# Kernel optimization log

Hardware: AMD Instinct MI355X
Metric: run time of the kernel (lower is better)

Reference implementation:

```python
import jax, jax.numpy as jnp
from jax import lax
import numpy as np

EPS = 1e-5


def ref_points(Hk, Wk):
    # torch linspace(0.5, Hk-0.5, Hk)/Hk * 2 - 1, stacked (y, x)
    ys = (jnp.linspace(0.5, Hk - 0.5, Hk) / Hk) * 2.0 - 1.0
    xs = (jnp.linspace(0.5, Wk - 0.5, Wk) / Wk) * 2.0 - 1.0
    yy, xx = jnp.meshgrid(ys, xs, indexing='ij')
    return jnp.stack([yy, xx], axis=-1)  # (Hk, Wk, 2) in (y, x) order


def grid_sample(img, grid):
    # Bilinear, align_corners=True, zeros padding (torch F.grid_sample defaults).
    # img: (N, C, Hi, Wi); grid: (N, Hg, Wg, 2) with (x, y) in [-1, 1].
    N, C, Hi, Wi = img.shape
    Hg, Wg = grid.shape[1], grid.shape[2]
    gx = (grid[..., 0] + 1.0) * 0.5 * (Wi - 1)
    gy = (grid[..., 1] + 1.0) * 0.5 * (Hi - 1)
    x0 = jnp.floor(gx)
    y0 = jnp.floor(gy)
    wx1 = gx - x0
    wy1 = gy - y0
    imgf = img.reshape(N, C, Hi * Wi)

    def corner(ix, iy, w):
        valid = (ix >= 0) & (ix < Wi) & (iy >= 0) & (iy < Hi)
        idx = (jnp.clip(iy, 0, Hi - 1).astype(jnp.int32) * Wi
               + jnp.clip(ix, 0, Wi - 1).astype(jnp.int32)).reshape(N, -1)
        vals = jax.vmap(lambda im, f: im[:, f])(imgf, idx)  # (N, C, Hg*Wg)
        return vals * (w * valid).reshape(N, 1, -1)

    out = (corner(x0, y0, (1 - wx1) * (1 - wy1))
           + corner(x0 + 1, y0, wx1 * (1 - wy1))
           + corner(x0, y0 + 1, (1 - wx1) * wy1)
           + corner(x0 + 1, y0 + 1, wx1 * wy1))
    return out.reshape(N, C, Hg, Wg)


def setup_inputs() -> dict:
    key = jax.random.key(0)
    ks = jax.random.split(key, 8)
    B, C, H, W = 8, 128, 64, 64
    gc, nH = 64, 4
    return {
        'x': jax.random.normal(ks[0], (B, C, H, W), jnp.float32),
        'w_dw': jax.random.normal(ks[1], (gc, 1, 5, 5), jnp.float32) * 0.1,
        'ln_w': jnp.ones((gc,), jnp.float32),
        'w_off': jax.random.normal(ks[2], (3, gc), jnp.float32) * 0.1,
        'wq': jax.random.normal(ks[3], (C, C), jnp.float32) * 0.05,
        'wk': jax.random.normal(ks[4], (C, C), jnp.float32) * 0.05,
        'wv': jax.random.normal(ks[5], (C, C), jnp.float32) * 0.05,
        'wo': jax.random.normal(ks[6], (C, C), jnp.float32) * 0.05,
        'rpe': jax.random.normal(ks[7], (nH, 2 * H - 1, 2 * W - 1), jnp.float32) * 0.01,
    }


def reference(x, w_dw, ln_w, w_off, wq, wk, wv, wo, rpe):
    B, C, H, W = x.shape
    G, nH = 2, 4
    gc = C // G           # group channels
    dh = C // nH          # head channels
    gh = nH // G          # heads per group
    scale = dh ** -0.5
    orf = 1.0             # offset_range_factor

    conv1x1 = lambda t, w: jnp.einsum('oi,bihw->bohw', w, t)

    q = conv1x1(x, wq)                                    # (B, C, H, W)
    q_off = q.reshape(B * G, gc, H, W)

    # conv_offset: depthwise 5x5 stride 4 pad 2 -> BiasFree LN (over C) -> GELU -> 1x1 to 3
    off = lax.conv_general_dilated(q_off, w_dw, (4, 4), ((2, 2), (2, 2)),
                                   dimension_numbers=('NCHW', 'OIHW', 'NCHW'),
                                   feature_group_count=gc)  # (B*G, gc, Hk, Wk)
    var = jnp.var(off, axis=1, keepdims=True)
    off = off / jnp.sqrt(var + EPS) * ln_w.reshape(1, -1, 1, 1)
    off = jax.nn.gelu(off, approximate=False)
    off = jnp.einsum('oi,bihw->bohw', w_off, off)          # (B*G, 3, Hk, Wk)

    Hk, Wk = off.shape[2], off.shape[3]
    n = Hk * Wk

    # channel 0 = y offset, channel 1 = x offset, channel 2 = modulation
    offset = jnp.stack([jnp.tanh(off[:, 0]) * (orf / Hk),
                        jnp.tanh(off[:, 1]) * (orf / Wk)], axis=-1)  # (B*G, Hk, Wk, 2) (y,x)
    dm = jax.nn.sigmoid(off[:, 2])[:, None]                # (B*G, 1, Hk, Wk)

    pos = offset + ref_points(Hk, Wk)[None]                # (B*G, Hk, Wk, 2) (y,x)

    xs = grid_sample(x.reshape(B * G, gc, H, W), pos[..., ::-1])  # grid in (x,y)
    xs = (xs * dm).reshape(B, C, 1, n)

    k = conv1x1(xs, wk).reshape(B * nH, dh, n)
    v = conv1x1(xs, wv).reshape(B * nH, dh, n)
    qf = q.reshape(B * nH, dh, H * W)

    attn = jnp.einsum('bcm,bcn->bmn', qf, k) * scale       # (B*nH, H*W, n)

    # relative-position bias sampled at continuous displacements
    rpe_b = jnp.broadcast_to(rpe[None], (B, nH, 2 * H - 1, 2 * W - 1)
                             ).reshape(B * G, gh, 2 * H - 1, 2 * W - 1)
    qg = ref_points(H, W).reshape(H * W, 2)                # (H*W, 2)
    disp = (qg[None, :, None, :] - pos.reshape(B * G, 1, n, 2)) * 0.5  # (B*G, H*W, n, 2)
    bias = grid_sample(rpe_b, disp[..., ::-1]).reshape(B * nH, H * W, n)

    attn = jax.nn.softmax(attn + bias, axis=2)
    out = jnp.einsum('bmn,bcn->bcm', attn, v).reshape(B, C, H, W)
    return conv1x1(out, wo)
```

## Files before the change

### kernel.cpp

```cpp
#include <hip/hip_runtime.h>
#include <hip/hip_bf16.h>
#include <math.h>

#define HW 4096
#define NCH 128

typedef __attribute__((ext_vector_type(8))) short short8;
typedef __attribute__((ext_vector_type(4))) float f32x4;
typedef __attribute__((ext_vector_type(4))) unsigned u32x4;

__device__ __forceinline__ short f2bf(float f) {
  union { __hip_bfloat16 h; short s; } u;
  u.h = __float2bfloat16(f);
  return u.s;
}
__device__ __forceinline__ float bf2f(short s) {
  union { unsigned u; float f; } u;
  u.u = ((unsigned)(unsigned short)s) << 16;
  return u.f;
}

__global__ __launch_bounds__(256) void xq_kernel(
    const float* __restrict__ x, const float* __restrict__ wq,
    const float* __restrict__ wk, const float* __restrict__ wv,
    const float* __restrict__ wo, const float* __restrict__ rpe,
    short* __restrict__ xT, float* __restrict__ qT,
    short* __restrict__ wk_bf, short* __restrict__ wv_bf,
    short* __restrict__ wo_bf, unsigned* __restrict__ tab) {
  __shared__ float s[128][65];
  int tid = threadIdx.x;
  if (blockIdx.y >= 8) {
    int id = (blockIdx.y - 8) * 64 + blockIdx.x;
    if (id < 64) {
      int i = id * 256 + tid;
      wk_bf[i] = f2bf(wk[i]);
      wv_bf[i] = f2bf(wv[i]);
      wo_bf[i] = f2bf(wo[i]);
    } else {
      int i = (id - 64) * 256 + tid;
      int h = i >> 14, r = i & 16383;
      int row = r >> 7, col = r & 127;
      float lo = 0.f, hi = 0.f;
      if (col < 127) {
        if (row >= 1) lo = rpe[h * 16129 + (row - 1) * 127 + col];
        if (row < 127) hi = rpe[h * 16129 + row * 127 + col];
      }
      union { unsigned u; _Float16 h2[2]; } pk;
      pk.h2[0] = (_Float16)(lo * 1.4426950408889634f);
      pk.h2[1] = (_Float16)((hi - lo) * 1.4426950408889634f);
      tab[i] = pk.u;
    }
    return;
  }
  int b = blockIdx.y;
  int m0 = blockIdx.x * 64;
  {
    int ml = tid & 63, ch = tid >> 6;
#pragma unroll
    for (int i = 0; i < 32; ++i) {
      int c = i * 4 + ch;
      s[c][ml] = x[((size_t)(b * NCH + c)) * HW + m0 + ml];
    }
  }
  __syncthreads();
  {
    int c = tid & 127, mh = tid >> 7;
#pragma unroll
    for (int i = 0; i < 32; ++i) {
      int m = i * 2 + mh;
      xT[((size_t)(b * HW + m0 + m)) * NCH + c] = f2bf(s[c][m]);
    }
  }
  int w = tid >> 6, lane = tid & 63, l15 = lane & 15, qd = lane >> 4;
  int mrow = w * 16 + l15;
  f32x4 acc[8];
#pragma unroll
  for (int ot = 0; ot < 8; ++ot) acc[ot] = (f32x4){0.f, 0.f, 0.f, 0.f};
#pragma unroll
  for (int kc = 0; kc < 4; ++kc) {
    short8 ah, al;
#pragma unroll
    for (int j = 0; j < 8; ++j) {
      float v = s[kc * 32 + qd * 8 + j][mrow];
      short hi = f2bf(v);
      ah[j] = hi;
      al[j] = f2bf(v - bf2f(hi));
    }
#pragma unroll
    for (int ot = 0; ot < 8; ++ot) {
      const float* wr = wq + (size_t)(ot * 16 + l15) * NCH + kc * 32 + qd * 8;
      f32x4 w0 = *(const f32x4*)wr;
      f32x4 w1 = *(const f32x4*)(wr + 4);
      short8 bh, bl;
#pragma unroll
      for (int j = 0; j < 4; ++j) {
        short h0 = f2bf(w0[j]);
        bh[j] = h0;
        bl[j] = f2bf(w0[j] - bf2f(h0));
        short h1 = f2bf(w1[j]);
        bh[4 + j] = h1;
        bl[4 + j] = f2bf(w1[j] - bf2f(h1));
      }
      acc[ot] = __builtin_amdgcn_mfma_f32_16x16x32_bf16(ah, bh, acc[ot], 0, 0, 0);
      acc[ot] = __builtin_amdgcn_mfma_f32_16x16x32_bf16(al, bh, acc[ot], 0, 0, 0);
      acc[ot] = __builtin_amdgcn_mfma_f32_16x16x32_bf16(ah, bl, acc[ot], 0, 0, 0);
    }
  }
#pragma unroll
  for (int ot = 0; ot < 8; ++ot)
#pragma unroll
    for (int r = 0; r < 4; ++r)
      qT[((size_t)(b * HW + m0 + w * 16 + qd * 4 + r)) * NCH + ot * 16 + l15] =
          acc[ot][r];
}

__device__ __forceinline__ float wsum64(float v) {
#pragma unroll
  for (int o = 32; o > 0; o >>= 1) v += __shfl_xor(v, o);
  return v;
}

__global__ __launch_bounds__(256) void conv_offset_kernel(
    const float* __restrict__ qT, const float* __restrict__ w_dw,
    const float* __restrict__ ln_w, const float* __restrict__ w_off,
    float* __restrict__ pos, float* __restrict__ dm) {
  int tid = threadIdx.x;
  int c = tid & 63;
  int p = blockIdx.x * 4 + (tid >> 6);
  int bg = blockIdx.y;
  int py = p >> 4, px = p & 15;
  const float* qp = qT + (size_t)(bg >> 1) * HW * NCH + (bg & 1) * 64 + c;
  const float* wd = w_dw + c * 25;
  float acc = 0.f;
#pragma unroll
  for (int ky = 0; ky < 5; ++ky) {
    int iy = 4 * py + ky - 2;
    if (iy < 0 || iy >= 64) continue;
#pragma unroll
    for (int kx = 0; kx < 5; ++kx) {
      int ix = 4 * px + kx - 2;
      if (ix < 0 || ix >= 64) continue;
      acc += wd[ky * 5 + kx] * qp[(size_t)(iy * 64 + ix) * NCH];
    }
  }
  float mean = wsum64(acc) * (1.f / 64.f);
  float msq = wsum64(acc * acc) * (1.f / 64.f);
  float var = msq - mean * mean;
  float g = acc * rsqrtf(var + 1e-5f) * ln_w[c];
  g = 0.5f * g * (1.f + erff(g * 0.70710678118654752f));
  float o0 = wsum64(w_off[c] * g);
  float o1 = wsum64(w_off[64 + c] * g);
  float o2 = wsum64(w_off[128 + c] * g);
  if (c == 0) {
    int idx = bg * 256 + p;
    pos[idx * 2] = tanhf(o0) * (1.f / 16.f) + ((py + 0.5f) * (1.f / 8.f) - 1.f);
    pos[idx * 2 + 1] = tanhf(o1) * (1.f / 16.f) + ((px + 0.5f) * (1.f / 8.f) - 1.f);
    dm[idx] = 1.f / (1.f + expf(-o2));
  }
}

__global__ __launch_bounds__(256) void sample_xs_kernel(
    const short* __restrict__ xT, const float* __restrict__ pos,
    const float* __restrict__ dm, short* __restrict__ xsT) {
  int tid = threadIdx.x;
  int c = tid & 63;
  int p = blockIdx.y * 4 + (tid >> 6);
  int bg = blockIdx.x;
  int b = bg >> 1, ch0 = (bg & 1) * 64;
  int idx = bg * 256 + p;
  float posy = pos[idx * 2], posx = pos[idx * 2 + 1];
  float dmv = dm[idx];
  float gx = (posx + 1.f) * 31.5f;
  float gy = (posy + 1.f) * 31.5f;
  float x0f = floorf(gx), y0f = floorf(gy);
  int ix = (int)x0f, iy = (int)y0f;
  float fx = gx - x0f, fy = gy - y0f;
  float w00 = (1.f - fx) * (1.f - fy), w10 = fx * (1.f - fy);
  float w01 = (1.f - fx) * fy, w11 = fx * fy;
  bool vx0 = (ix >= 0 && ix < 64), vx1 = (ix + 1 >= 0 && ix + 1 < 64);
  bool vy0 = (iy >= 0 && iy < 64), vy1 = (iy + 1 >= 0 && iy + 1 < 64);
  if (!(vx0 && vy0)) w00 = 0.f;
  if (!(vx1 && vy0)) w10 = 0.f;
  if (!(vx0 && vy1)) w01 = 0.f;
  if (!(vx1 && vy1)) w11 = 0.f;
  int x0c = min(max(ix, 0), 63), x1c = min(max(ix + 1, 0), 63);
  int y0c = min(max(iy, 0), 63), y1c = min(max(iy + 1, 0), 63);
  size_t rb = (size_t)b * HW * NCH + ch0 + c;
  float v = w00 * bf2f(xT[rb + (size_t)(y0c * 64 + x0c) * NCH]) +
            w10 * bf2f(xT[rb + (size_t)(y0c * 64 + x1c) * NCH]) +
            w01 * bf2f(xT[rb + (size_t)(y1c * 64 + x0c) * NCH]) +
            w11 * bf2f(xT[rb + (size_t)(y1c * 64 + x1c) * NCH]);
  xsT[((size_t)(b * 256 + p)) * NCH + ch0 + c] = f2bf(v * dmv);
}

__global__ __launch_bounds__(256) void kv_mfma_kernel(
    const short* __restrict__ xsT, const short* __restrict__ wk_bf,
    const short* __restrict__ wv_bf, short* __restrict__ kbf,
    short* __restrict__ vbf) {
  int tid = threadIdx.x;
  int w = tid >> 6, lane = tid & 63, l15 = lane & 15, qd = lane >> 4;
  int bh = blockIdx.x, b = bh >> 2;
  int n0 = blockIdx.y * 64 + w * 16;
  f32x4 acc[2];
  acc[0] = (f32x4){0.f, 0.f, 0.f, 0.f};
  acc[1] = (f32x4){0.f, 0.f, 0.f, 0.f};

  size_t xrow = ((size_t)(b * 256 + n0 + l15)) * NCH + qd * 8;
  if (blockIdx.z == 0) {
#pragma unroll
    for (int kc = 0; kc < 4; ++kc) {
      short8 a = *(const short8*)&xsT[xrow + kc * 32];
#pragma unroll
      for (int ot = 0; ot < 2; ++ot) {
        short8 bb = *(const short8*)&wk_bf[(size_t)((bh & 3) * 32 + ot * 16 + l15) * NCH + kc * 32 + qd * 8];
        acc[ot] = __builtin_amdgcn_mfma_f32_16x16x32_bf16(a, bb, acc[ot], 0, 0, 0);
      }
    }
#pragma unroll
    for (int ot = 0; ot < 2; ++ot)
#pragma unroll
      for (int r = 0; r < 4; ++r)
        kbf[((size_t)(bh * 256 + n0 + qd * 4 + r)) * 32 + ot * 16 + l15] =
            f2bf(acc[ot][r]);
  } else {
#pragma unroll
    for (int kc = 0; kc < 4; ++kc) {
      short8 bb = *(const short8*)&xsT[xrow + kc * 32];
#pragma unroll
      for (int ot = 0; ot < 2; ++ot) {
        short8 a = *(const short8*)&wv_bf[(size_t)((bh & 3) * 32 + ot * 16 + l15) * NCH + kc * 32 + qd * 8];
        acc[ot] = __builtin_amdgcn_mfma_f32_16x16x32_bf16(a, bb, acc[ot], 0, 0, 0);
      }
    }
#pragma unroll
    for (int ot = 0; ot < 2; ++ot)
#pragma unroll
      for (int r = 0; r < 4; ++r)
        vbf[((size_t)(bh * 32 + ot * 16 + qd * 4 + r)) * 256 + n0 + l15] =
            f2bf(acc[ot][r]);
  }
}

#define PROW 264
#define TROWS 66

struct __attribute__((packed)) upair { unsigned lo, hi; };

__global__ __launch_bounds__(256, 4) void attn_kernel(
    const float* __restrict__ qT, const short* __restrict__ kbf,
    const short* __restrict__ vbf, const float* __restrict__ pos,
    const unsigned* __restrict__ tabg, short* __restrict__ outT) {
  __shared__ __align__(16) unsigned s_tab[TROWS * 128];
  __shared__ __align__(16) float s_pxs[256];
  __shared__ __align__(16) unsigned s_fyrow[256];
  short* s_p = (short*)s_tab;

  int tid = threadIdx.x;
  int wv = tid >> 6;
  int lane = tid & 63;
  int l15 = lane & 15;
  int qd = lane >> 4;
  int bh = blockIdx.y;
  int b = bh >> 2, h = bh & 3;
  int bg = b * 2 + (h >> 1);
  int m0 = blockIdx.x * 64 + wv * 16;

  float ry = ((float)blockIdx.x + 0.5f) * (1.f / 32.f) - 1.f;
  float gy0 = 63.f + ry * 31.5f;
  int row0 = (int)floorf(gy0) - 32;

  {
    const uint4* src = (const uint4*)(tabg + (size_t)h * 16384 + row0 * 128);
    uint4* dst = (uint4*)s_tab;
#pragma unroll
    for (int i = 0; i < 8; ++i)
      __builtin_amdgcn_global_load_lds(
          (const __attribute__((address_space(1))) void*)(src + i * 256 + tid),
          (__attribute__((address_space(3))) void*)(dst + i * 256 + tid), 16,
          0, 0);
    if (tid < 64)
      __builtin_amdgcn_global_load_lds(
          (const __attribute__((address_space(1))) void*)(src + 2048 + tid),
          (__attribute__((address_space(3))) void*)(dst + 2048 + tid), 16,
          0, 0);
  }
  {
    float2 p2 = ((const float2*)(pos + (size_t)bg * 512))[tid];
    float gyb = gy0 - (float)row0 + 1.f;
    float gy = gyb - p2.x * 31.5f;
    float y0f = floorf(gy);
    union { unsigned short us; _Float16 hh; } fyp;
    fyp.hh = (_Float16)(gy - y0f);
    unsigned rowoff = ((unsigned)(int)y0f) << 7;
    s_pxs[tid] = p2.y * 31.5f;
    s_fyrow[tid] = (rowoff << 16) | (unsigned)fyp.us;
  }

  short8 qfrag;
  {
    const float* qg = qT + ((size_t)(b * HW + m0 + l15)) * NCH + h * 32 + qd * 8;
    f32x4 a0 = *(const f32x4*)qg;
    f32x4 a1 = *(const f32x4*)(qg + 4);
#pragma unroll
    for (int j = 0; j < 4; ++j) {
      qfrag[j] = f2bf(a0[j]);
      qfrag[4 + j] = f2bf(a1[j]);
    }
  }

  f32x4 acc[16];
  {
    const short* kb = kbf + ((size_t)bh * 256 + l15) * 32 + qd * 8;
#pragma unroll
    for (int t = 0; t < 16; ++t) {
      short8 kf = *(const short8*)(kb + t * 16 * 32);
      acc[t] = __builtin_amdgcn_mfma_f32_16x16x32_bf16(
          kf, qfrag, (f32x4){0.f, 0.f, 0.f, 0.f}, 0, 0, 0);
    }
  }
  __syncthreads();

  int m = m0 + l15;
  float gx0 = ((((float)(m & 63) + 0.5f) * (1.f / 32.f) - 1.f) * 0.5f + 1.f) * 63.f;

  float sm = 0.f;
#pragma unroll
  for (int t = 0; t < 16; ++t) {
    int nb = t * 16 + qd * 4;
    f32x4 pxs4 = *(const f32x4*)&s_pxs[nb];
    u32x4 fr4 = *(const u32x4*)&s_fyrow[nb];
#pragma unroll
    for (int r = 0; r < 4; ++r) {
      float gx = gx0 - pxs4[r];
      float x0f = floorf(gx);
      float fx = gx - x0f;
      int xl = (int)x0f;
      unsigned fr = fr4[r];
      int ai = (int)(fr >> 16) + xl;
      upair pr = *(const upair*)(s_tab + ai);
      union { unsigned u; _Float16 h2[2]; } L, R;
      union { unsigned short us; _Float16 hh; } F;
      L.u = pr.lo;
      R.u = pr.hi;
      F.us = (unsigned short)(fr & 0xffffu);
      _Float16 fy16 = F.hh;
      _Float16 fx16 = (_Float16)fx;
      _Float16 bL = L.h2[0] + fy16 * L.h2[1];
      _Float16 bR = R.h2[0] + fy16 * R.h2[1];
      _Float16 b16 = bL + fx16 * (bR - bL);
      float bias = (float)b16;
      float e = exp2f(fmaf(acc[t][r], 0.25503486121880191f, bias));
      acc[t][r] = e;
      sm += e;
    }
  }
  sm += __shfl_xor(sm, 16);
  sm += __shfl_xor(sm, 32);
  float inv = 1.f / sm;

  __syncthreads();

  const short* vb = vbf + ((size_t)bh * 32 + l15) * 256 + qd * 8;
  short8 v0p[4], v1p[4];
#pragma unroll
  for (int j = 0; j < 4; ++j) {
    v0p[j] = *(const short8*)(vb + j * 32);
    v1p[j] = *(const short8*)(vb + 16 * 256 + j * 32);
  }

  {
    short* pw = s_p + wv * 16 * PROW + l15 * PROW;
#pragma unroll
    for (int t = 0; t < 16; ++t) {
      short4 pk;
      pk.x = f2bf(acc[t][0]);
      pk.y = f2bf(acc[t][1]);
      pk.z = f2bf(acc[t][2]);
      pk.w = f2bf(acc[t][3]);
      *(short4*)(pw + t * 16 + qd * 4) = pk;
    }
  }

  f32x4 o0 = {0.f, 0.f, 0.f, 0.f}, o1 = {0.f, 0.f, 0.f, 0.f};
  {
    const short* prd = s_p + wv * 16 * PROW + l15 * PROW + qd * 8;
#pragma unroll
    for (int ch = 0; ch < 8; ++ch) {
      short8 pf = *(const short8*)(prd + ch * 32);
      short8 v0c = v0p[ch & 3];
      short8 v1c = v1p[ch & 3];
      if (ch + 4 < 8) {
        v0p[ch & 3] = *(const short8*)(vb + (ch + 4) * 32);
        v1p[ch & 3] = *(const short8*)(vb + 16 * 256 + (ch + 4) * 32);
      }
      o0 = __builtin_amdgcn_mfma_f32_16x16x32_bf16(v0c, pf, o0, 0, 0, 0);
      o1 = __builtin_amdgcn_mfma_f32_16x16x32_bf16(v1c, pf, o1, 0, 0, 0);
    }
  }
  {
    size_t row = (size_t)(b * HW + m0 + l15) * NCH + h * 32 + qd * 4;
    short4 s0, s1;
    s0.x = f2bf(o0[0] * inv); s0.y = f2bf(o0[1] * inv);
    s0.z = f2bf(o0[2] * inv); s0.w = f2bf(o0[3] * inv);
    s1.x = f2bf(o1[0] * inv); s1.y = f2bf(o1[1] * inv);
    s1.z = f2bf(o1[2] * inv); s1.w = f2bf(o1[3] * inv);
    *(short4*)&outT[row] = s0;
    *(short4*)&outT[row + 16] = s1;
  }
}

__global__ __launch_bounds__(256) void wo_mfma_kernel(
    const short* __restrict__ attnT, const short* __restrict__ wo_bf,
    float* __restrict__ out) {
  int tid = threadIdx.x;
  int wv = tid >> 6;
  int lane = tid & 63;
  int l15 = lane & 15;
  int qd = lane >> 4;
  int b = blockIdx.x >> 6;
  int m0 = (blockIdx.x & 63) * 64 + wv * 16;

  f32x4 acc[8];
#pragma unroll
  for (int ot = 0; ot < 8; ++ot) acc[ot] = (f32x4){0.f, 0.f, 0.f, 0.f};

  const short* arow = attnT + (size_t)(b * HW + m0 + l15) * NCH + qd * 8;
  const short* wrow = wo_bf + (size_t)l15 * NCH + qd * 8;
#pragma unroll
  for (int kc = 0; kc < 4; ++kc) {
    short8 afrag = *(const short8*)(arow + kc * 32);
#pragma unroll
    for (int ot = 0; ot < 8; ++ot) {
      short8 bfrag = *(const short8*)(wrow + (size_t)ot * 16 * NCH + kc * 32);
      acc[ot] = __builtin_amdgcn_mfma_f32_16x16x32_bf16(afrag, bfrag, acc[ot],
                                                        0, 0, 0);
    }
  }
#pragma unroll
  for (int ot = 0; ot < 8; ++ot) {
    float* op = out + ((size_t)b * NCH + ot * 16 + l15) * HW + m0 + qd * 4;
    *(f32x4*)op = acc[ot];
  }
}

extern "C" void kernel_launch(void* const* d_in, const int* in_sizes, int n_in,
                              void* d_out, int out_size, void* d_ws,
                              size_t ws_size, hipStream_t stream) {
  const float* x = (const float*)d_in[0];
  const float* w_dw = (const float*)d_in[1];
  const float* ln_w = (const float*)d_in[2];
  const float* w_off = (const float*)d_in[3];
  const float* wq = (const float*)d_in[4];
  const float* wk = (const float*)d_in[5];
  const float* wv = (const float*)d_in[6];
  const float* wo = (const float*)d_in[7];
  const float* rpe = (const float*)d_in[8];
  float* out = (float*)d_out;

  float* qT = out;
  short* sb = (short*)d_ws;
  short* xT = sb;
  short* outT = sb;
  short* xsT = sb + 4194304;
  short* kbf = sb + 4456448;
  short* vbf = sb + 4718592;
  short* wk_bf = sb + 4980736;
  short* wv_bf = sb + 4997120;
  short* wo_bf = sb + 5013504;
  unsigned* tab = (unsigned*)(sb + 5029888);
  float* pos = (float*)(sb + 5160960);
  float* dm = pos + 8192;

  xq_kernel<<<dim3(64, 13), 256, 0, stream>>>(x, wq, wk, wv, wo, rpe, xT, qT,
                                              wk_bf, wv_bf, wo_bf, tab);
  conv_offset_kernel<<<dim3(64, 16), 256, 0, stream>>>(qT, w_dw, ln_w, w_off,
                                                       pos, dm);
  sample_xs_kernel<<<dim3(16, 64), 256, 0, stream>>>(xT, pos, dm, xsT);
  kv_mfma_kernel<<<dim3(32, 4, 2), 256, 0, stream>>>(xsT, wk_bf, wv_bf, kbf,
                                                     vbf);
  attn_kernel<<<dim3(64, 32), 256, 0, stream>>>(qT, kbf, vbf, pos, tab, outT);
  wo_mfma_kernel<<<512, 256, 0, stream>>>(outT, wo_bf, out);
}
```

Before: 162.9 us.

## Fuse offset conv with sampling and split attention keys across two wave groups

Merges the offset-prediction kernel and the bilinear sampling kernel into one, so the sampling uses the computed positions straight from registers. This removes a launch and a global round trip for pos/dm. The attention kernel now runs 512 threads per block, with two wave groups each handling half of the 256 keys. Their partial softmax sums and PV accumulators are combined through shared memory, which costs extra barriers and LDS traffic in exchange for more parallelism and fewer registers per thread.

Result: slower. 167.2 us (+2.7%).

```diff
diff --git a/kernel.cpp b/kernel.cpp
--- a/kernel.cpp
+++ b/kernel.cpp
@@ -120,10 +120,11 @@
   return v;
 }
 
-__global__ __launch_bounds__(256) void conv_offset_kernel(
+__global__ __launch_bounds__(256) void conv_sample_kernel(
     const float* __restrict__ qT, const float* __restrict__ w_dw,
     const float* __restrict__ ln_w, const float* __restrict__ w_off,
-    float* __restrict__ pos, float* __restrict__ dm) {
+    const short* __restrict__ xT, float* __restrict__ pos,
+    float* __restrict__ dm, short* __restrict__ xsT) {
   int tid = threadIdx.x;
   int c = tid & 63;
   int p = blockIdx.x * 4 + (tid >> 6);
@@ -151,25 +152,16 @@
   float o0 = wsum64(w_off[c] * g);
   float o1 = wsum64(w_off[64 + c] * g);
   float o2 = wsum64(w_off[128 + c] * g);
+  int idx = bg * 256 + p;
+  float posy = tanhf(o0) * (1.f / 16.f) + ((py + 0.5f) * (1.f / 8.f) - 1.f);
+  float posx = tanhf(o1) * (1.f / 16.f) + ((px + 0.5f) * (1.f / 8.f) - 1.f);
+  float dmv = 1.f / (1.f + expf(-o2));
   if (c == 0) {
-    int idx = bg * 256 + p;
-    pos[idx * 2] = tanhf(o0) * (1.f / 16.f) + ((py + 0.5f) * (1.f / 8.f) - 1.f);
-    pos[idx * 2 + 1] = tanhf(o1) * (1.f / 16.f) + ((px + 0.5f) * (1.f / 8.f) - 1.f);
-    dm[idx] = 1.f / (1.f + expf(-o2));
-  }
-}
-
-__global__ __launch_bounds__(256) void sample_xs_kernel(
-    const short* __restrict__ xT, const float* __restrict__ pos,
-    const float* __restrict__ dm, short* __restrict__ xsT) {
-  int tid = threadIdx.x;
-  int c = tid & 63;
-  int p = blockIdx.y * 4 + (tid >> 6);
-  int bg = blockIdx.x;
+    pos[idx * 2] = posy;
+    pos[idx * 2 + 1] = posx;
+    dm[idx] = dmv;
+  }
   int b = bg >> 1, ch0 = (bg & 1) * 64;
-  int idx = bg * 256 + p;
-  float posy = pos[idx * 2], posx = pos[idx * 2 + 1];
-  float dmv = dm[idx];
   float gx = (posx + 1.f) * 31.5f;
   float gy = (posy + 1.f) * 31.5f;
   float x0f = floorf(gx), y0f = floorf(gy);
@@ -246,24 +238,28 @@
 
 struct __attribute__((packed)) upair { unsigned lo, hi; };
 
-__global__ __launch_bounds__(256, 4) void attn_kernel(
+__global__ __launch_bounds__(512, 8) void attn_kernel(
     const float* __restrict__ qT, const short* __restrict__ kbf,
     const short* __restrict__ vbf, const float* __restrict__ pos,
     const unsigned* __restrict__ tabg, short* __restrict__ outT) {
   __shared__ __align__(16) unsigned s_tab[TROWS * 128];
   __shared__ __align__(16) float s_pxs[256];
   __shared__ __align__(16) unsigned s_fyrow[256];
+  __shared__ __align__(16) float s_sm[128];
   short* s_p = (short*)s_tab;
+  float* s_comb = (float*)s_tab;
 
   int tid = threadIdx.x;
   int wv = tid >> 6;
+  int mt = wv & 3;
+  int nh = wv >> 2;
   int lane = tid & 63;
   int l15 = lane & 15;
   int qd = lane >> 4;
   int bh = blockIdx.y;
   int b = bh >> 2, h = bh & 3;
   int bg = b * 2 + (h >> 1);
-  int m0 = blockIdx.x * 64 + wv * 16;
+  int m0 = blockIdx.x * 64 + mt * 16;
 
   float ry = ((float)blockIdx.x + 0.5f) * (1.f / 32.f) - 1.f;
   float gy0 = 63.f + ry * 31.5f;
@@ -273,10 +269,10 @@
     const uint4* src = (const uint4*)(tabg + (size_t)h * 16384 + row0 * 128);
     uint4* dst = (uint4*)s_tab;
 #pragma unroll
-    for (int i = 0; i < 8; ++i)
+    for (int i = 0; i < 4; ++i)
       __builtin_amdgcn_global_load_lds(
-          (const __attribute__((address_space(1))) void*)(src + i * 256 + tid),
-          (__attribute__((address_space(3))) void*)(dst + i * 256 + tid), 16,
+          (const __attribute__((address_space(1))) void*)(src + i * 512 + tid),
+          (__attribute__((address_space(3))) void*)(dst + i * 512 + tid), 16,
           0, 0);
     if (tid < 64)
       __builtin_amdgcn_global_load_lds(
@@ -284,7 +280,7 @@
           (__attribute__((address_space(3))) void*)(dst + 2048 + tid), 16,
           0, 0);
   }
-  {
+  if (tid < 256) {
     float2 p2 = ((const float2*)(pos + (size_t)bg * 512))[tid];
     float gyb = gy0 - (float)row0 + 1.f;
     float gy = gyb - p2.x * 31.5f;
@@ -308,13 +304,14 @@
     }
   }
 
-  f32x4 acc[16];
+  f32x4 acc[8];
   {
     const short* kb = kbf + ((size_t)bh * 256 + l15) * 32 + qd * 8;
 #pragma unroll
-    for (int t = 0; t < 16; ++t) {
+    for (int tt = 0; tt < 8; ++tt) {
+      int t = nh * 8 + tt;
       short8 kf = *(const short8*)(kb + t * 16 * 32);
-      acc[t] = __builtin_amdgcn_mfma_f32_16x16x32_bf16(
+      acc[tt] = __builtin_amdgcn_mfma_f32_16x16x32_bf16(
           kf, qfrag, (f32x4){0.f, 0.f, 0.f, 0.f}, 0, 0, 0);
     }
   }
@@ -325,8 +322,8 @@
 
   float sm = 0.f;
 #pragma unroll
-  for (int t = 0; t < 16; ++t) {
-    int nb = t * 16 + qd * 4;
+  for (int tt = 0; tt < 8; ++tt) {
+    int nb = (nh * 8 + tt) * 16 + qd * 4;
     f32x4 pxs4 = *(const f32x4*)&s_pxs[nb];
     u32x4 fr4 = *(const u32x4*)&s_fyrow[nb];
 #pragma unroll
@@ -349,61 +346,64 @@
       _Float16 bR = R.h2[0] + fy16 * R.h2[1];
       _Float16 b16 = bL + fx16 * (bR - bL);
       float bias = (float)b16;
-      float e = exp2f(fmaf(acc[t][r], 0.25503486121880191f, bias));
-      acc[t][r] = e;
+      float e = exp2f(fmaf(acc[tt][r], 0.25503486121880191f, bias));
+      acc[tt][r] = e;
       sm += e;
     }
   }
   sm += __shfl_xor(sm, 16);
   sm += __shfl_xor(sm, 32);
-  float inv = 1.f / sm;
 
   __syncthreads();
 
-  const short* vb = vbf + ((size_t)bh * 32 + l15) * 256 + qd * 8;
-  short8 v0p[4], v1p[4];
-#pragma unroll
-  for (int j = 0; j < 4; ++j) {
-    v0p[j] = *(const short8*)(vb + j * 32);
-    v1p[j] = *(const short8*)(vb + 16 * 256 + j * 32);
-  }
-
-  {
-    short* pw = s_p + wv * 16 * PROW + l15 * PROW;
-#pragma unroll
-    for (int t = 0; t < 16; ++t) {
+  {
+    short* pw = s_p + mt * 16 * PROW + l15 * PROW;
+#pragma unroll
+    for (int tt = 0; tt < 8; ++tt) {
       short4 pk;
-      pk.x = f2bf(acc[t][0]);
-      pk.y = f2bf(acc[t][1]);
-      pk.z = f2bf(acc[t][2]);
-      pk.w = f2bf(acc[t][3]);
-      *(short4*)(pw + t * 16 + qd * 4) = pk;
-    }
-  }
+      pk.x = f2bf(acc[tt][0]);
+      pk.y = f2bf(acc[tt][1]);
+      pk.z = f2bf(acc[tt][2]);
+      pk.w = f2bf(acc[tt][3]);
+      *(short4*)(pw + (nh * 8 + tt) * 16 + qd * 4) = pk;
+    }
+  }
+  if (qd == 0) s_sm[wv * 16 + l15] = sm;
 
   f32x4 o0 = {0.f, 0.f, 0.f, 0.f}, o1 = {0.f, 0.f, 0.f, 0.f};
   {
-    const short* prd = s_p + wv * 16 * PROW + l15 * PROW + qd * 8;
-#pragma unroll
-    for (int ch = 0; ch < 8; ++ch) {
+    const short* vb = vbf + ((size_t)bh * 32 + l15) * 256 + qd * 8;
+    const short* prd = s_p + mt * 16 * PROW + l15 * PROW + qd * 8;
+#pragma unroll
+    for (int cc = 0; cc < 4; ++cc) {
+      int ch = nh * 4 + cc;
       short8 pf = *(const short8*)(prd + ch * 32);
-      short8 v0c = v0p[ch & 3];
-      short8 v1c = v1p[ch & 3];
-      if (ch + 4 < 8) {
-        v0p[ch & 3] = *(const short8*)(vb + (ch + 4) * 32);
-        v1p[ch & 3] = *(const short8*)(vb + 16 * 256 + (ch + 4) * 32);
-      }
-      o0 = __builtin_amdgcn_mfma_f32_16x16x32_bf16(v0c, pf, o0, 0, 0, 0);
-      o1 = __builtin_amdgcn_mfma_f32_16x16x32_bf16(v1c, pf, o1, 0, 0, 0);
-    }
-  }
-  {
+      short8 v0 = *(const short8*)(vb + ch * 32);
+      short8 v1 = *(const short8*)(vb + 16 * 256 + ch * 32);
+      o0 = __builtin_amdgcn_mfma_f32_16x16x32_bf16(v0, pf, o0, 0, 0, 0);
+      o1 = __builtin_amdgcn_mfma_f32_16x16x32_bf16(v1, pf, o1, 0, 0, 0);
+    }
+  }
+  __syncthreads();
+
+  if (nh == 1) {
+    float* cb = s_comb + ((size_t)(mt * 16 + l15)) * 36 + qd * 4;
+    *(f32x4*)cb = o0;
+    *(f32x4*)(cb + 16) = o1;
+  }
+  __syncthreads();
+
+  if (nh == 0) {
+    float inv = 1.f / (sm + s_sm[(wv ^ 4) * 16 + l15]);
+    const float* cb = s_comb + ((size_t)(mt * 16 + l15)) * 36 + qd * 4;
+    f32x4 p0 = *(const f32x4*)cb;
+    f32x4 p1 = *(const f32x4*)(cb + 16);
     size_t row = (size_t)(b * HW + m0 + l15) * NCH + h * 32 + qd * 4;
     short4 s0, s1;
-    s0.x = f2bf(o0[0] * inv); s0.y = f2bf(o0[1] * inv);
-    s0.z = f2bf(o0[2] * inv); s0.w = f2bf(o0[3] * inv);
-    s1.x = f2bf(o1[0] * inv); s1.y = f2bf(o1[1] * inv);
-    s1.z = f2bf(o1[2] * inv); s1.w = f2bf(o1[3] * inv);
+    s0.x = f2bf((o0[0] + p0[0]) * inv); s0.y = f2bf((o0[1] + p0[1]) * inv);
+    s0.z = f2bf((o0[2] + p0[2]) * inv); s0.w = f2bf((o0[3] + p0[3]) * inv);
+    s1.x = f2bf((o1[0] + p1[0]) * inv); s1.y = f2bf((o1[1] + p1[1]) * inv);
+    s1.z = f2bf((o1[2] + p1[2]) * inv); s1.w = f2bf((o1[3] + p1[3]) * inv);
     *(short4*)&outT[row] = s0;
     *(short4*)&outT[row + 16] = s1;
   }
@@ -473,11 +473,10 @@
 
   xq_kernel<<<dim3(64, 13), 256, 0, stream>>>(x, wq, wk, wv, wo, rpe, xT, qT,
                                               wk_bf, wv_bf, wo_bf, tab);
-  conv_offset_kernel<<<dim3(64, 16), 256, 0, stream>>>(qT, w_dw, ln_w, w_off,
-                                                       pos, dm);
-  sample_xs_kernel<<<dim3(16, 64), 256, 0, stream>>>(xT, pos, dm, xsT);
+  conv_sample_kernel<<<dim3(64, 16), 256, 0, stream>>>(qT, w_dw, ln_w, w_off,
+                                                       xT, pos, dm, xsT);
   kv_mfma_kernel<<<dim3(32, 4, 2), 256, 0, stream>>>(xsT, wk_bf, wv_bf, kbf,
                                                      vbf);
-  attn_kernel<<<dim3(64, 32), 256, 0, stream>>>(qT, kbf, vbf, pos, tab, outT);
+  attn_kernel<<<dim3(64, 32), 512, 0, stream>>>(qT, kbf, vbf, pos, tab, outT);
   wo_mfma_kernel<<<512, 256, 0, stream>>>(outT, wo_bf, out);
 }
```
